# Kernel tuning notes

Measured on AMD Instinct MI355X. Metric: run time of the kernel, lower is better.

The kernel has to match this reference:

```python
import jax, jax.numpy as jnp
import numpy as np

B, S, D = 8, 512, 1024
E, F, K = 8, 4096, 2


def setup_inputs() -> dict:
    key = jax.random.key(0)
    ks = jax.random.split(key, 8)
    scale = 1.0 / np.sqrt(D)
    return {
        "x": jax.random.normal(ks[0], (B, S, D), jnp.float32),
        "y": jax.random.randint(ks[1], (B,), 0, D),
        "W": jax.random.normal(ks[2], (D, D), jnp.float32) * scale,
        "b": jnp.zeros((D,), jnp.float32),
        "Wg": jax.random.normal(ks[3], (D, E), jnp.float32) * scale,
        "w1": jax.random.normal(ks[4], (E, D, F), jnp.float32) * scale,
        "b1": jnp.zeros((E, F), jnp.float32),
        "w2": jax.random.normal(ks[5], (E, F, D), jnp.float32) * (1.0 / np.sqrt(F)),
        "b2": jnp.zeros((E, D), jnp.float32),
    }


def reference(x, y, W, b, Wg, w1, b1, w2, b2):
    # linear projection (torch Linear convention: x @ W.T + b)
    lin = jnp.einsum("bsd,ed->bse", x, W) + b                      # [B,S,D]

    # --- MoE: top-2 softmax gate, renormalized over the top-k ---
    gate_logits = jnp.einsum("bsd,de->bse", lin, Wg)               # [B,S,E]
    probs = jax.nn.softmax(gate_logits, axis=-1)
    top_p, top_i = jax.lax.top_k(probs, K)                          # [B,S,K]
    top_p = top_p / jnp.sum(top_p, axis=-1, keepdims=True)
    # combine weights per expert: scatter top-k probs back to [B,S,E]
    gate = jnp.sum(jax.nn.one_hot(top_i, E, dtype=lin.dtype) * top_p[..., None], axis=-2)  # [B,S,E]

    # expert FFNs evaluated densely, combined by (sparse) gate weights
    h = jax.nn.relu(jnp.einsum("bsd,edf->ebsf", lin, w1) + b1[:, None, None, :])  # [E,B,S,F]
    expert_out = jnp.einsum("ebsf,efd->ebsd", h, w2) + b2[:, None, None, :]        # [E,B,S,D]
    moe_out = jnp.einsum("bse,ebsd->bsd", gate, expert_out)                        # [B,S,D]

    # residual, mean pool over sequence, cross-entropy
    sent_emb = jnp.mean(x + moe_out, axis=1)                       # [B,D] used as logits
    logp = jax.nn.log_softmax(sent_emb, axis=-1)
    loss = -jnp.mean(logp[jnp.arange(B), y])
    return loss
```

## Files before the change

kernel.cpp:

```cpp
#include <hip/hip_runtime.h>

#define TOK 4096
#define DD  1024
#define NE  8
#define FF  4096
#define NB  8
#define SS  512
#define HROWS 8320

typedef unsigned short ushort_t;
typedef __attribute__((ext_vector_type(8))) short bshort8;
typedef __attribute__((ext_vector_type(4))) float floatx4;

__device__ __forceinline__ ushort_t f2bf(float f) {
  unsigned int u = __float_as_uint(f);
  u += 0x7fffu + ((u >> 16) & 1u);
  return (ushort_t)(u >> 16);
}
__device__ __forceinline__ float bf2f(ushort_t h) {
  return __uint_as_float(((unsigned int)h) << 16);
}

__device__ __forceinline__ void gl_lds16(const ushort_t* g, ushort_t* l) {
  __builtin_amdgcn_global_load_lds(
      (const __attribute__((address_space(1))) unsigned int*)g,
      (__attribute__((address_space(3))) unsigned int*)l, 16, 0, 0);
}

__global__ __launch_bounds__(256) void k_cast(
    const float* __restrict__ in, ushort_t* __restrict__ out, int n4) {
  int i = blockIdx.x * 256 + threadIdx.x;
  if (i < n4) {
    float4 v = ((const float4*)in)[i];
    ushort4 o;
    o.x = f2bf(v.x); o.y = f2bf(v.y); o.z = f2bf(v.z); o.w = f2bf(v.w);
    ((ushort4*)out)[i] = o;
  }
}

__global__ __launch_bounds__(256) void k_transpose_cast(
    const float* __restrict__ in, size_t in_estride, int in_rstride,
    ushort_t* __restrict__ out, size_t out_estride, int out_rstride) {
  __shared__ ushort_t t[64][70];
  const float* ib = in + blockIdx.z * in_estride;
  ushort_t* ob = out + blockIdx.z * out_estride;
  const int r0 = blockIdx.y * 64, c0 = blockIdx.x * 64;
  const int tid = threadIdx.x;
  const int lr = tid >> 4, lc4 = (tid & 15) * 4;
#pragma unroll
  for (int it = 0; it < 4; ++it) {
    int r = lr + it * 16;
    float4 v = *(const float4*)&ib[(size_t)(r0 + r) * in_rstride + c0 + lc4];
    t[r][lc4 + 0] = f2bf(v.x);
    t[r][lc4 + 1] = f2bf(v.y);
    t[r][lc4 + 2] = f2bf(v.z);
    t[r][lc4 + 3] = f2bf(v.w);
  }
  __syncthreads();
  const int oc = tid >> 5, od2 = (tid & 31) * 2;
#pragma unroll
  for (int it = 0; it < 8; ++it) {
    int cc = oc + it * 8;
    ushort2 w;
    w.x = t[od2 + 0][cc];
    w.y = t[od2 + 1][cc];
    *(ushort2*)&ob[(size_t)(c0 + cc) * out_rstride + r0 + od2] = w;
  }
}

__global__ __launch_bounds__(256) void k_mfma0(
    const ushort_t* __restrict__ A, const ushort_t* __restrict__ Bm,
    const float* __restrict__ bias, ushort_t* __restrict__ Obf, int kext) {
  const int gx = gridDim.x, gy = gridDim.y;
  int flat = blockIdx.x + gx * blockIdx.y;
  const int nwg = gx * gy;
  flat = (flat & 7) * (nwg >> 3) + (flat >> 3);
  const int bx = flat % gx;
  const int by = flat / gx;

  const int m0 = by * 128;
  const int n0 = bx * 128;

  __shared__ ushort_t Als[3][128 * 32];
  __shared__ ushort_t Bls[3][128 * 32];

  const int tid = threadIdx.x;
  const int lane = tid & 63;
  const int w = tid >> 6;
  const int wm = (w & 1) * 64, wn = (w >> 1) * 64;
  const int lm = lane & 15, lq = lane >> 4;
  const int sr = lane >> 2;
  const int sg = lane & 3;

  const int r0 = w * 32 + sr;
  const int r1 = r0 + 16;
  const int q = (sg - (r0 >> 1)) & 3;
  const int d0 = r0 * 32 + sg * 8;
  const int d1 = r1 * 32 + sg * 8;
  const ushort_t* sA0 = A + (size_t)(m0 + r0) * kext + q * 8;
  const ushort_t* sA1 = A + (size_t)(m0 + r1) * kext + q * 8;
  const ushort_t* sB0 = Bm + (size_t)(n0 + r0) * kext + q * 8;
  const ushort_t* sB1 = Bm + (size_t)(n0 + r1) * kext + q * 8;

#define STG0(bi, kt)                           \
  do {                                         \
    const int ko_ = (kt) << 5;                 \
    gl_lds16(sA0 + ko_, &Als[bi][d0]);         \
    gl_lds16(sA1 + ko_, &Als[bi][d1]);         \
    gl_lds16(sB0 + ko_, &Bls[bi][d0]);         \
    gl_lds16(sB1 + ko_, &Bls[bi][d1]);         \
  } while (0)

  floatx4 zero = {0.f, 0.f, 0.f, 0.f};
  floatx4 acc[4][4];
#pragma unroll
  for (int i = 0; i < 4; ++i)
#pragma unroll
    for (int j = 0; j < 4; ++j) acc[i][j] = zero;

  const int nk = kext >> 5;

  STG0(0, 0);
  STG0(1, 1);
  asm volatile("s_waitcnt vmcnt(4)" ::: "memory");
  asm volatile("s_barrier" ::: "memory");

  int cur = 0;
  for (int k = 0; k < nk; ++k) {
    const ushort_t* Ab = Als[cur];
    const ushort_t* Bb = Bls[cur];
    bshort8 af[4], bfr[4];
#pragma unroll
    for (int i = 0; i < 4; ++i) {
      int r = wm + i * 16 + lm;
      af[i] = *(const bshort8*)&Ab[r * 32 + (((lq + (r >> 1)) & 3) * 8)];
    }
#pragma unroll
    for (int j = 0; j < 4; ++j) {
      int r = wn + j * 16 + lm;
      bfr[j] = *(const bshort8*)&Bb[r * 32 + (((lq + (r >> 1)) & 3) * 8)];
    }
    int pf = cur + 2; if (pf >= 3) pf -= 3;
    if (k + 2 < nk) STG0(pf, k + 2);

    asm volatile("s_waitcnt lgkmcnt(0)" ::: "memory");
    __builtin_amdgcn_sched_barrier(0);

#pragma unroll
    for (int i = 0; i < 4; ++i)
#pragma unroll
      for (int j = 0; j < 4; ++j)
        acc[i][j] = __builtin_amdgcn_mfma_f32_16x16x32_bf16(af[i], bfr[j],
                                                            acc[i][j], 0, 0, 0);

    if (k + 1 < nk) {
      if (k + 2 < nk) {
        asm volatile("s_waitcnt vmcnt(4)" ::: "memory");
      } else {
        asm volatile("s_waitcnt vmcnt(0)" ::: "memory");
      }
      asm volatile("s_barrier" ::: "memory");
    }
    cur += 1; if (cur >= 3) cur -= 3;
  }
#undef STG0

#pragma unroll
  for (int i = 0; i < 4; ++i) {
#pragma unroll
    for (int j = 0; j < 4; ++j) {
      int n = wn + j * 16 + lm;
#pragma unroll
      for (int rr = 0; rr < 4; ++rr) {
        int m = wm + i * 16 + lq * 4 + rr;
        float v = acc[i][j][rr];
        int gn = n0 + n;
        v += bias[gn];
        Obf[(size_t)(m0 + m) * DD + gn] = f2bf(v);
      }
    }
  }
}

template <int MODE>
__global__ __launch_bounds__(512, 4) void k_mg(
    const ushort_t* __restrict__ A, const ushort_t* __restrict__ Bm,
    const float* __restrict__ bias, ushort_t* __restrict__ Obf,
    float* __restrict__ Of, const int* __restrict__ cnt,
    const int* __restrict__ offs, const int* __restrict__ btok, int f0,
    int accum, int kext, int ast, int ost, size_t bstride) {
  const int gx = gridDim.x, gy = gridDim.y;
  int flat = blockIdx.x + gx * (blockIdx.y + gy * blockIdx.z);
  const int nwg = gx * gy * (int)gridDim.z;
  flat = (flat & 7) * (nwg >> 3) + (flat >> 3);
  const int bx = flat % gx;
  const int t2 = flat / gx;
  const int by = t2 % gy;
  const int bz = t2 / gy;

  const int e = bz;
  const int c = cnt[e];
  const int off = offs[e];
  if (by * 256 >= c) return;
  const int m0 = by * 256;
  const int n0 = bx * 128;
  const ushort_t* Bp = Bm + (size_t)e * bstride;

  __shared__ ushort_t Als[3][256 * 32];
  __shared__ ushort_t Bls[3][128 * 32];
  __shared__ int ts[256];

  const int tid = threadIdx.x;
  if (tid < 256) {
    int p = m0 + tid;
    int r;
    if (MODE == 1) r = btok[e * TOK + min(p, c - 1)];
    else r = off + min(p, c - 1);
    ts[tid] = r;
  }
  __syncthreads();

  const int lane = tid & 63;
  const int w = tid >> 6;
  const int wm = (w >> 1) * 64;
  const int wn = (w & 1) * 64;
  const int lm = lane & 15, lq = lane >> 4;
  const int sr = lane >> 2;
  const int sg = lane & 3;

  const int ra0 = w * 16 + sr;
  const int ra1 = 128 + ra0;
  const int q = (sg - (ra0 >> 1)) & 3;
  const int dA0 = ra0 * 32 + sg * 8;
  const int dA1 = ra1 * 32 + sg * 8;
  const ushort_t* sA0 = A + (size_t)ts[ra0] * ast + q * 8;
  const ushort_t* sA1 = A + (size_t)ts[ra1] * ast + q * 8;
  const ushort_t* sB0 = Bp + (size_t)(n0 + ra0) * kext + q * 8;

#define STG(bi, kt)                            \
  do {                                         \
    const int ko_ = (kt) << 5;                 \
    gl_lds16(sA0 + ko_, &Als[bi][dA0]);        \
    gl_lds16(sA1 + ko_, &Als[bi][dA1]);        \
    gl_lds16(sB0 + ko_, &Bls[bi][dA0]);        \
  } while (0)

  floatx4 zero = {0.f, 0.f, 0.f, 0.f};
  floatx4 acc[4][4];
#pragma unroll
  for (int i = 0; i < 4; ++i)
#pragma unroll
    for (int j = 0; j < 4; ++j) acc[i][j] = zero;

  const int nk = kext >> 5;

  STG(0, 0);
  STG(1, 1);
  asm volatile("s_waitcnt vmcnt(3)" ::: "memory");
  asm volatile("s_barrier" ::: "memory");

  int cur = 0;
  for (int k = 0; k < nk; ++k) {
    const ushort_t* Ab = Als[cur];
    const ushort_t* Bb = Bls[cur];
    bshort8 af[4], bfr[4];
#pragma unroll
    for (int i = 0; i < 4; ++i) {
      int r = wm + i * 16 + lm;
      af[i] = *(const bshort8*)&Ab[r * 32 + (((lq + (r >> 1)) & 3) * 8)];
    }
#pragma unroll
    for (int j = 0; j < 4; ++j) {
      int r = wn + j * 16 + lm;
      bfr[j] = *(const bshort8*)&Bb[r * 32 + (((lq + (r >> 1)) & 3) * 8)];
    }
    int pf = cur + 2; if (pf >= 3) pf -= 3;
    if (k + 2 < nk) STG(pf, k + 2);

    asm volatile("s_waitcnt lgkmcnt(0)" ::: "memory");
    __builtin_amdgcn_sched_barrier(0);

#pragma unroll
    for (int i = 0; i < 4; ++i)
#pragma unroll
      for (int j = 0; j < 4; ++j)
        acc[i][j] = __builtin_amdgcn_mfma_f32_16x16x32_bf16(af[i], bfr[j],
                                                            acc[i][j], 0, 0, 0);

    if (k + 1 < nk) {
      if (k + 2 < nk) {
        asm volatile("s_waitcnt vmcnt(3)" ::: "memory");
      } else {
        asm volatile("s_waitcnt vmcnt(0)" ::: "memory");
      }
      asm volatile("s_barrier" ::: "memory");
    }
    cur += 1; if (cur >= 3) cur -= 3;
  }
#undef STG

#pragma unroll
  for (int i = 0; i < 4; ++i) {
#pragma unroll
    for (int j = 0; j < 4; ++j) {
      const int n = wn + j * 16 + lm;
#pragma unroll
      for (int rr = 0; rr < 4; ++rr) {
        const int m = wm + i * 16 + lq * 4 + rr;
        float v = acc[i][j][rr];
        const int p = m0 + m;
        if (p < c) {
          const int gn = n0 + n;
          if (MODE == 1) {
            v += bias[(size_t)e * FF + f0 + gn];
            v = fmaxf(v, 0.f);
            Obf[(size_t)(off + p) * ost + gn] = f2bf(v);
          } else {
            if (!accum) v += bias[(size_t)e * DD + gn];
            float* dp = &Of[(size_t)(off + p) * DD + gn];
            if (accum) *dp += v; else *dp = v;
          }
        }
      }
    }
  }
}

__global__ __launch_bounds__(256) void k_logits(
    const ushort_t* __restrict__ lin_bf, const float* __restrict__ Wg,
    int* __restrict__ topi, float* __restrict__ wts) {
  const int wv = threadIdx.x >> 6, lane = threadIdx.x & 63;
  const int t = blockIdx.x * 4 + wv;
  float acc[NE] = {};
  const ushort_t* lr = lin_bf + (size_t)t * DD;
#pragma unroll 4
  for (int d0 = 0; d0 < DD; d0 += 64) {
    float v = bf2f(lr[d0 + lane]);
    const float* wgr = Wg + (size_t)(d0 + lane) * NE;
    float4 g0 = *(const float4*)(wgr);
    float4 g1 = *(const float4*)(wgr + 4);
    acc[0] += v * g0.x; acc[1] += v * g0.y; acc[2] += v * g0.z; acc[3] += v * g0.w;
    acc[4] += v * g1.x; acc[5] += v * g1.y; acc[6] += v * g1.z; acc[7] += v * g1.w;
  }
#pragma unroll
  for (int off = 32; off > 0; off >>= 1) {
#pragma unroll
    for (int e = 0; e < NE; ++e) acc[e] += __shfl_xor(acc[e], off);
  }
  if (lane == 0) {
    int i1 = 0;
#pragma unroll
    for (int e = 1; e < NE; ++e)
      if (acc[e] > acc[i1]) i1 = e;
    int i2 = (i1 == 0) ? 1 : 0;
#pragma unroll
    for (int e = 0; e < NE; ++e)
      if (e != i1 && acc[e] > acc[i2]) i2 = e;
    float r = __expf(acc[i2] - acc[i1]);
    topi[t] = i1 | (i2 << 4);
    wts[2 * t + 0] = 1.0f / (1.0f + r);
    wts[2 * t + 1] = r / (1.0f + r);
  }
}

#define RT 512
__global__ __launch_bounds__(RT) void k_route(
    const int* __restrict__ topi, int* __restrict__ cnt, int* __restrict__ offs,
    int* __restrict__ btok, int* __restrict__ eslot) {
  __shared__ int sc[NE][RT + 1];
  __shared__ int tot[NE];
  const int tid = threadIdx.x;
  int lc[NE] = {};
  int my[8];
#pragma unroll
  for (int i = 0; i < 8; ++i) {
    int t = tid * 8 + i;
    int p = topi[t];
    my[i] = p;
    lc[p & 15]++;
    lc[(p >> 4) & 15]++;
  }
#pragma unroll
  for (int e = 0; e < NE; ++e) sc[e][tid] = lc[e];
  __syncthreads();
  if (tid < NE) {
    int s = 0;
    for (int i = 0; i < RT; ++i) { int v = sc[tid][i]; sc[tid][i] = s; s += v; }
    tot[tid] = s;
  }
  __syncthreads();
  if (tid == 0) {
    int s = 0;
    for (int e = 0; e < NE; ++e) { offs[e] = s; cnt[e] = tot[e]; s += tot[e]; }
  }
  __syncthreads();
  int run[NE];
#pragma unroll
  for (int e = 0; e < NE; ++e) run[e] = sc[e][tid];
#pragma unroll
  for (int i = 0; i < 8; ++i) {
    int t = tid * 8 + i, p = my[i];
    int e1 = p & 15, e2 = (p >> 4) & 15;
    int s1 = run[e1]++;
    btok[e1 * TOK + s1] = t;
    eslot[2 * t + 0] = e1 * TOK + s1;
    int s2 = run[e2]++;
    btok[e2 * TOK + s2] = t;
    eslot[2 * t + 1] = e2 * TOK + s2;
  }
}

__global__ __launch_bounds__(256) void k_pool(
    const float* __restrict__ x, const float* __restrict__ ob,
    const int* __restrict__ offs, const int* __restrict__ eslot,
    const float* __restrict__ wts, float* __restrict__ sent) {
  const int b = blockIdx.y;
  const int d = blockIdx.x * 256 + threadIdx.x;
  const int sc = blockIdx.z;
  float a = 0.f;
  for (int s = sc * 64; s < sc * 64 + 64; ++s) {
    int t = b * SS + s;
    int e0 = eslot[2 * t], e1 = eslot[2 * t + 1];
    int g0 = offs[e0 >> 12] + (e0 & (TOK - 1));
    int g1 = offs[e1 >> 12] + (e1 & (TOK - 1));
    a += x[(size_t)t * DD + d] + wts[2 * t] * ob[(size_t)g0 * DD + d] +
         wts[2 * t + 1] * ob[(size_t)g1 * DD + d];
  }
  atomicAdd(&sent[b * DD + d], a * (1.0f / SS));
}

__global__ __launch_bounds__(1024) void k_loss(
    const float* __restrict__ sent, const int* __restrict__ y,
    float* __restrict__ out) {
  __shared__ float red[16];
  const int tid = threadIdx.x;
  const int lane = tid & 63, wv = tid >> 6;
  float loss = 0.f;
  for (int b = 0; b < NB; ++b) {
    float v = sent[b * DD + tid];
    float m = v;
#pragma unroll
    for (int off = 32; off > 0; off >>= 1) m = fmaxf(m, __shfl_xor(m, off));
    if (lane == 0) red[wv] = m;
    __syncthreads();
    float m2 = red[0];
#pragma unroll
    for (int w = 1; w < 16; ++w) m2 = fmaxf(m2, red[w]);
    __syncthreads();
    float ex = __expf(v - m2);
#pragma unroll
    for (int off = 32; off > 0; off >>= 1) ex += __shfl_xor(ex, off);
    if (lane == 0) red[wv] = ex;
    __syncthreads();
    if (tid == 0) {
      float se = 0.f;
      for (int w = 0; w < 16; ++w) se += red[w];
      loss += m2 + logf(se) - sent[b * DD + y[b]];
    }
    __syncthreads();
  }
  if (tid == 0) out[0] = loss / NB;
}

extern "C" void kernel_launch(void* const* d_in, const int* in_sizes, int n_in,
                              void* d_out, int out_size, void* d_ws,
                              size_t ws_size, hipStream_t stream) {
  const float* x  = (const float*)d_in[0];
  const int*   y  = (const int*)d_in[1];
  const float* W  = (const float*)d_in[2];
  const float* bb = (const float*)d_in[3];
  const float* Wg = (const float*)d_in[4];
  const float* w1 = (const float*)d_in[5];
  const float* b1 = (const float*)d_in[6];
  const float* w2 = (const float*)d_in[7];
  const float* b2 = (const float*)d_in[8];
  float* out = (float*)d_out;

  auto need = [](size_t FCr) -> size_t {
    size_t o = 0;
    auto al = [&](size_t b) { o = (o + b + 255) & ~255ull; };
    al((size_t)TOK * DD * 2);
    al((size_t)TOK * DD * 2);
    al((size_t)DD * DD * 2);
    al((size_t)HROWS * FCr * 2);
    al((size_t)NE * FCr * DD * 2);
    al((size_t)NE * DD * FCr * 2);
    al((size_t)HROWS * DD * 4);
    al((size_t)NE * TOK * 4);
    al(64); al(64);
    al((size_t)TOK * 4);
    al((size_t)2 * TOK * 4);
    al((size_t)2 * TOK * 4);
    al((size_t)NB * DD * 4);
    return o;
  };
  const int nchunks = (ws_size >= need(FF)) ? 1 : 4;
  const int FCr = FF / nchunks;

  char* base = (char*)d_ws;
  size_t o = 0;
  auto al = [&](size_t b) -> char* {
    char* p = base + o;
    o = (o + b + 255) & ~255ull;
    return p;
  };
  ushort_t* lin_bf = (ushort_t*)al((size_t)TOK * DD * 2);
  ushort_t* x_bf   = (ushort_t*)al((size_t)TOK * DD * 2);
  ushort_t* W_bf   = (ushort_t*)al((size_t)DD * DD * 2);
  ushort_t* h_bf   = (ushort_t*)al((size_t)HROWS * FCr * 2);
  ushort_t* w1t    = (ushort_t*)al((size_t)NE * FCr * DD * 2);
  ushort_t* w2t    = (ushort_t*)al((size_t)NE * DD * FCr * 2);
  float*    ob     = (float*)al((size_t)HROWS * DD * 4);
  int*      btok   = (int*)al((size_t)NE * TOK * 4);
  int*      cnt    = (int*)al(64);
  int*      offs   = (int*)al(64);
  int*      topi   = (int*)al((size_t)TOK * 4);
  int*      eslot  = (int*)al((size_t)2 * TOK * 4);
  float*    wts    = (float*)al((size_t)2 * TOK * 4);
  float*    sent   = (float*)al((size_t)NB * DD * 4);

  hipMemsetAsync(sent, 0, NB * DD * sizeof(float), stream);

  k_cast<<<TOK * DD / 4 / 256, 256, 0, stream>>>(x, x_bf, TOK * DD / 4);
  k_cast<<<DD * DD / 4 / 256, 256, 0, stream>>>(W, W_bf, DD * DD / 4);

  k_mfma0<<<dim3(DD / 128, TOK / 128), 256, 0, stream>>>(
      x_bf, W_bf, bb, lin_bf, DD);

  k_logits<<<TOK / 4, 256, 0, stream>>>(lin_bf, Wg, topi, wts);
  k_route<<<1, RT, 0, stream>>>(topi, cnt, offs, btok, eslot);

  for (int ci = 0; ci < nchunks; ++ci) {
    int f0 = ci * FCr;
    k_transpose_cast<<<dim3(FCr / 64, DD / 64, NE), 256, 0, stream>>>(
        w1 + f0, (size_t)DD * FF, FF, w1t, (size_t)FCr * DD, DD);
    k_mg<1><<<dim3(FCr / 128, TOK / 256, NE), 512, 0, stream>>>(
        lin_bf, w1t, b1, h_bf, nullptr, cnt, offs, btok, f0, 0,
        DD, DD, FCr, (size_t)FCr * DD);
    k_transpose_cast<<<dim3(DD / 64, FCr / 64, NE), 256, 0, stream>>>(
        w2 + (size_t)f0 * DD, (size_t)FF * DD, DD, w2t, (size_t)DD * FCr, FCr);
    k_mg<2><<<dim3(DD / 128, TOK / 256, NE), 512, 0, stream>>>(
        h_bf, w2t, b2, nullptr, ob, cnt, offs, btok, f0, ci > 0 ? 1 : 0,
        FCr, FCr, DD, (size_t)DD * FCr);
  }

  k_pool<<<dim3(DD / 256, NB, 8), 256, 0, stream>>>(x, ob, offs, eslot, wts,
                                                    sent);
  k_loss<<<1, 1024, 0, stream>>>(sent, y, out);
}
```

Before: 599.8 us.

## Split-K the second expert GEMM and widen transpose-cast stores

```diff
diff --git a/kernel.cpp b/kernel.cpp
--- a/kernel.cpp
+++ b/kernel.cpp
@@ -10,6 +10,7 @@
 
 typedef unsigned short ushort_t;
 typedef __attribute__((ext_vector_type(8))) short bshort8;
+typedef __attribute__((ext_vector_type(8))) unsigned short ushortx8;
 typedef __attribute__((ext_vector_type(4))) float floatx4;
 
 __device__ __forceinline__ ushort_t f2bf(float f) {
@@ -57,14 +58,15 @@
     t[r][lc4 + 3] = f2bf(v.w);
   }
   __syncthreads();
-  const int oc = tid >> 5, od2 = (tid & 31) * 2;
-#pragma unroll
-  for (int it = 0; it < 8; ++it) {
-    int cc = oc + it * 8;
-    ushort2 w;
-    w.x = t[od2 + 0][cc];
-    w.y = t[od2 + 1][cc];
-    *(ushort2*)&ob[(size_t)(c0 + cc) * out_rstride + r0 + od2] = w;
+  const int oc = tid >> 3;
+  const int org = (tid & 7) * 8;
+#pragma unroll
+  for (int it = 0; it < 2; ++it) {
+    int cc = oc + it * 32;
+    ushortx8 wv;
+#pragma unroll
+    for (int j = 0; j < 8; ++j) wv[j] = t[org + j][cc];
+    *(ushortx8*)&ob[(size_t)(c0 + cc) * out_rstride + r0 + org] = wv;
   }
 }
 
@@ -188,7 +190,8 @@
     const float* __restrict__ bias, ushort_t* __restrict__ Obf,
     float* __restrict__ Of, const int* __restrict__ cnt,
     const int* __restrict__ offs, const int* __restrict__ btok, int f0,
-    int accum, int kext, int ast, int ost, size_t bstride) {
+    int accum, int kext, int klen, int ast, int ost, size_t bstride,
+    float* __restrict__ Ofx) {
   const int gx = gridDim.x, gy = gridDim.y;
   int flat = blockIdx.x + gx * (blockIdx.y + gy * blockIdx.z);
   const int nwg = gx * gy * (int)gridDim.z;
@@ -198,7 +201,9 @@
   const int by = t2 % gy;
   const int bz = t2 / gy;
 
-  const int e = bz;
+  const int e = bz & (NE - 1);
+  const int sk = bz >> 3;
+  const int koff = sk * klen;
   const int c = cnt[e];
   const int off = offs[e];
   if (by * 256 >= c) return;
@@ -233,9 +238,9 @@
   const int q = (sg - (ra0 >> 1)) & 3;
   const int dA0 = ra0 * 32 + sg * 8;
   const int dA1 = ra1 * 32 + sg * 8;
-  const ushort_t* sA0 = A + (size_t)ts[ra0] * ast + q * 8;
-  const ushort_t* sA1 = A + (size_t)ts[ra1] * ast + q * 8;
-  const ushort_t* sB0 = Bp + (size_t)(n0 + ra0) * kext + q * 8;
+  const ushort_t* sA0 = A + (size_t)ts[ra0] * ast + koff + q * 8;
+  const ushort_t* sA1 = A + (size_t)ts[ra1] * ast + koff + q * 8;
+  const ushort_t* sB0 = Bp + (size_t)(n0 + ra0) * kext + koff + q * 8;
 
 #define STG(bi, kt)                            \
   do {                                         \
@@ -252,7 +257,7 @@
 #pragma unroll
     for (int j = 0; j < 4; ++j) acc[i][j] = zero;
 
-  const int nk = kext >> 5;
+  const int nk = klen >> 5;
 
   STG(0, 0);
   STG(1, 1);
@@ -316,9 +321,13 @@
             v = fmaxf(v, 0.f);
             Obf[(size_t)(off + p) * ost + gn] = f2bf(v);
           } else {
-            if (!accum) v += bias[(size_t)e * DD + gn];
-            float* dp = &Of[(size_t)(off + p) * DD + gn];
-            if (accum) *dp += v; else *dp = v;
+            if (sk) {
+              Ofx[(size_t)(off + p) * DD + gn] = v;
+            } else {
+              if (!accum) v += bias[(size_t)e * DD + gn];
+              float* dp = &Of[(size_t)(off + p) * DD + gn];
+              if (accum) *dp += v; else *dp = v;
+            }
           }
         }
       }
@@ -412,6 +421,7 @@
 
 __global__ __launch_bounds__(256) void k_pool(
     const float* __restrict__ x, const float* __restrict__ ob,
+    const float* __restrict__ obx, int usesk,
     const int* __restrict__ offs, const int* __restrict__ eslot,
     const float* __restrict__ wts, float* __restrict__ sent) {
   const int b = blockIdx.y;
@@ -423,8 +433,13 @@
     int e0 = eslot[2 * t], e1 = eslot[2 * t + 1];
     int g0 = offs[e0 >> 12] + (e0 & (TOK - 1));
     int g1 = offs[e1 >> 12] + (e1 & (TOK - 1));
-    a += x[(size_t)t * DD + d] + wts[2 * t] * ob[(size_t)g0 * DD + d] +
-         wts[2 * t + 1] * ob[(size_t)g1 * DD + d];
+    float o0 = ob[(size_t)g0 * DD + d];
+    float o1 = ob[(size_t)g1 * DD + d];
+    if (usesk) {
+      o0 += obx[(size_t)g0 * DD + d];
+      o1 += obx[(size_t)g1 * DD + d];
+    }
+    a += x[(size_t)t * DD + d] + wts[2 * t] * o0 + wts[2 * t + 1] * o1;
   }
   atomicAdd(&sent[b * DD + d], a * (1.0f / SS));
 }
@@ -519,6 +534,9 @@
   float*    wts    = (float*)al((size_t)2 * TOK * 4);
   float*    sent   = (float*)al((size_t)NB * DD * 4);
 
+  float* obx = (float*)w1t;
+  const int usesk = (nchunks == 1) ? 1 : 0;
+
   hipMemsetAsync(sent, 0, NB * DD * sizeof(float), stream);
 
   k_cast<<<TOK * DD / 4 / 256, 256, 0, stream>>>(x, x_bf, TOK * DD / 4);
@@ -536,15 +554,16 @@
         w1 + f0, (size_t)DD * FF, FF, w1t, (size_t)FCr * DD, DD);
     k_mg<1><<<dim3(FCr / 128, TOK / 256, NE), 512, 0, stream>>>(
         lin_bf, w1t, b1, h_bf, nullptr, cnt, offs, btok, f0, 0,
-        DD, DD, FCr, (size_t)FCr * DD);
+        DD, DD, DD, FCr, (size_t)FCr * DD, ob);
     k_transpose_cast<<<dim3(DD / 64, FCr / 64, NE), 256, 0, stream>>>(
         w2 + (size_t)f0 * DD, (size_t)FF * DD, DD, w2t, (size_t)DD * FCr, FCr);
-    k_mg<2><<<dim3(DD / 128, TOK / 256, NE), 512, 0, stream>>>(
+    k_mg<2><<<dim3(DD / 128, TOK / 256, NE * (usesk ? 2 : 1)), 512, 0,
+              stream>>>(
         h_bf, w2t, b2, nullptr, ob, cnt, offs, btok, f0, ci > 0 ? 1 : 0,
-        FCr, FCr, DD, (size_t)DD * FCr);
-  }
-
-  k_pool<<<dim3(DD / 256, NB, 8), 256, 0, stream>>>(x, ob, offs, eslot, wts,
-                                                    sent);
+        FCr, usesk ? FCr / 2 : FCr, FCr, DD, (size_t)DD * FCr, obx);
+  }
+
+  k_pool<<<dim3(DD / 256, NB, 8), 256, 0, stream>>>(x, ob, obx, usesk, offs,
+                                                    eslot, wts, sent);
   k_loss<<<1, 1024, 0, stream>>>(sent, y, out);
 }
```

Result: slower. 643.9 us (+7.3%).
